# Optimization experiments

Hardware: AMD Instinct MI355X
Metric: run time of the kernel (lower is better)

Reference implementation:

```python
import jax, jax.numpy as jnp
import numpy as np


def quat2mat(q):
    # q: [B,4] in (w,x,y,z) order; normalize then standard rotation matrix.
    q = q / jnp.linalg.norm(q, axis=-1, keepdims=True)
    w, x, y, z = q[:, 0], q[:, 1], q[:, 2], q[:, 3]
    R = jnp.stack([
        1 - 2 * (y * y + z * z), 2 * (x * y - w * z), 2 * (x * z + w * y),
        2 * (x * y + w * z), 1 - 2 * (x * x + z * z), 2 * (y * z - w * x),
        2 * (x * z - w * y), 2 * (y * z + w * x), 1 - 2 * (x * x + y * y),
    ], axis=-1).reshape(-1, 3, 3)
    return R


def setup_inputs() -> dict:
    key = jax.random.key(0)
    k1, k2, k3, k4, k5 = jax.random.split(key, 5)
    B, N = 32, 2048
    return {
        "q_est": jax.random.normal(k1, (B, 4), dtype=jnp.float32),
        "q_gt": jax.random.normal(k2, (B, 4), dtype=jnp.float32),
        "T": jax.random.normal(k3, (B, 3), dtype=jnp.float32),
        "pts": jax.random.normal(k4, (B, N, 3), dtype=jnp.float32),
        "symmetries": jax.random.randint(k5, (B, 1), 0, 2, dtype=jnp.int32),
    }


def reference(q_est, q_gt, T, pts, symmetries):
    # ego=False path: T unused.
    B = pts.shape[0]
    N = pts.shape[1]
    sym = symmetries.reshape(-1).astype(bool)  # [B]

    R_est = quat2mat(q_est)  # [B,3,3]
    R_gt = quat2mat(q_gt)

    pts_t = jnp.transpose(pts, (0, 2, 1))        # [B,3,N]
    pts_est = R_est @ pts_t                       # [B,3,N]
    pts_gt = R_gt @ pts_t                         # [B,3,N]

    # PLoss per-point squared distances: [B,N]
    d_p = jnp.sum((pts_est - pts_gt) ** 2, axis=1)

    # SLoss: pairwise squared dists via bmm decomposition, then min over gt points.
    x = jnp.transpose(pts_est, (0, 2, 1))  # [B,N,3]
    y = jnp.transpose(pts_gt, (0, 2, 1))   # [B,N,3]
    xx = jnp.sum(x * x, axis=-1)           # [B,N] (diag of x x^T)
    yy = jnp.sum(y * y, axis=-1)           # [B,N]
    zz = jnp.einsum('bnd,bmd->bnm', x, y)  # [B,N,N]
    P = xx[:, :, None] + yy[:, None, :] - 2.0 * zz
    d_s = jnp.min(P, axis=2)               # [B,N]

    # num_sym * s_loss / size + num_non_sym * p_loss / size simplifies to
    # (masked_sum_s + masked_sum_p) / (2 * N * B); num_sym/num_non_sym cancel.
    sum_s = jnp.sum(jnp.where(sym[:, None], d_s, 0.0))
    sum_p = jnp.sum(jnp.where(sym[:, None], 0.0, d_p))
    return (sum_s + sum_p) / (2.0 * N * B)
```

## Files before the change

kernel.cpp:

```cpp
#include <hip/hip_runtime.h>


#define TPB  256
#define NPTS 2048
#define MS   16
#define MCH  (NPTS / MS)
#define PX   8

__device__ __forceinline__ void quat2mat(const float* __restrict__ q, float R[9]) {
    float w = q[0], x = q[1], y = q[2], z = q[3];
    float inv = 1.0f / sqrtf(w*w + x*x + y*y + z*z);
    w *= inv; x *= inv; y *= inv; z *= inv;
    R[0] = 1.f - 2.f*(y*y + z*z); R[1] = 2.f*(x*y - w*z);       R[2] = 2.f*(x*z + w*y);
    R[3] = 2.f*(x*y + w*z);       R[4] = 1.f - 2.f*(x*x + z*z); R[5] = 2.f*(y*z - w*x);
    R[6] = 2.f*(x*z - w*y);       R[7] = 2.f*(y*z + w*x);       R[8] = 1.f - 2.f*(x*x + y*y);
}

__device__ __forceinline__ float block_reduce_add(float v, float* red) {
    #pragma unroll
    for (int off = 32; off > 0; off >>= 1)
        v += __shfl_down(v, off, 64);
    const int tid = threadIdx.x;
    if ((tid & 63) == 0) red[tid >> 6] = v;
    __syncthreads();
    return red[0] + red[1] + red[2] + red[3];
}

__global__ __launch_bounds__(TPB) void pts_loss_A(
    const float* __restrict__ q_est, const float* __restrict__ q_gt,
    const float* __restrict__ pts, const int* __restrict__ symmetries,
    float* __restrict__ out, float* __restrict__ partial,
    float* __restrict__ bsum)
{
    const int b   = blockIdx.x;
    const int ms  = blockIdx.y;
    const int tid = threadIdx.x;

    __shared__ float4 ybuf[MCH];
    __shared__ float  red[TPB / 64];

    if (b == 0 && ms == 0 && tid == 0) *out = 0.f;

    const bool is_sym = symmetries[b] != 0;
    const float* pb = pts + (size_t)b * NPTS * 3;

    if (!is_sym) {
        if (ms != 0) return;
        float Re[9], Rg[9];
        quat2mat(q_est + 4*b, Re);
        quat2mat(q_gt  + 4*b, Rg);
        float s = 0.f;
        #pragma unroll
        for (int k = 0; k < PX; ++k) {
            int n = k * TPB + tid;
            float p0 = pb[3*n+0], p1 = pb[3*n+1], p2 = pb[3*n+2];
            float d0 = (Re[0]-Rg[0])*p0 + (Re[1]-Rg[1])*p1 + (Re[2]-Rg[2])*p2;
            float d1 = (Re[3]-Rg[3])*p0 + (Re[4]-Rg[4])*p1 + (Re[5]-Rg[5])*p2;
            float d2 = (Re[6]-Rg[6])*p0 + (Re[7]-Rg[7])*p1 + (Re[8]-Rg[8])*p2;
            s += d0*d0 + d1*d1 + d2*d2;
        }
        s = block_reduce_add(s, red);
        if (tid == 0) bsum[b] = s;
        return;
    }

    float Re[9], Rg[9];
    quat2mat(q_est + 4*b, Re);
    quat2mat(q_gt  + 4*b, Rg);

    if (tid < MCH) {
        int m = ms * MCH + tid;
        float p0 = pb[3*m+0], p1 = pb[3*m+1], p2 = pb[3*m+2];
        float y0 = Rg[0]*p0 + Rg[1]*p1 + Rg[2]*p2;
        float y1 = Rg[3]*p0 + Rg[4]*p1 + Rg[5]*p2;
        float y2 = Rg[6]*p0 + Rg[7]*p1 + Rg[8]*p2;
        ybuf[tid] = make_float4(y0, y1, y2, y0*y0 + y1*y1 + y2*y2);
    }
    __syncthreads();

    float nx0[PX], nx1[PX], nx2[PX], xx[PX], mins[PX];
    #pragma unroll
    for (int k = 0; k < PX; ++k) {
        int n = k * TPB + tid;
        float p0 = pb[3*n+0], p1 = pb[3*n+1], p2 = pb[3*n+2];
        float x0 = Re[0]*p0 + Re[1]*p1 + Re[2]*p2;
        float x1 = Re[3]*p0 + Re[4]*p1 + Re[5]*p2;
        float x2 = Re[6]*p0 + Re[7]*p1 + Re[8]*p2;
        nx0[k] = -2.f*x0; nx1[k] = -2.f*x1; nx2[k] = -2.f*x2;
        xx[k]  = x0*x0 + x1*x1 + x2*x2;
        mins[k] = 1e30f;
    }

    #pragma unroll 4
    for (int m = 0; m < MCH; ++m) {
        float4 y = ybuf[m];
        #pragma unroll
        for (int k = 0; k < PX; ++k) {
            float t = fmaf(nx0[k], y.x, fmaf(nx1[k], y.y, fmaf(nx2[k], y.z, y.w)));
            mins[k] = fminf(mins[k], t);
        }
    }

    float* pp = partial + ((size_t)b * MS + ms) * NPTS;
    #pragma unroll
    for (int k = 0; k < PX; ++k)
        pp[k * TPB + tid] = mins[k] + xx[k];
}

__global__ __launch_bounds__(TPB) void pts_loss_B(
    const int* __restrict__ symmetries,
    const float* __restrict__ partial,
    const float* __restrict__ bsum, float* __restrict__ out, float scale)
{
    const int b   = blockIdx.x;
    const int tid = threadIdx.x;
    __shared__ float red[TPB / 64];

    if (symmetries[b] == 0) {
        if (tid == 0) atomicAdd(out, bsum[b] * scale);
        return;
    }

    const float* pb = partial + (size_t)b * MS * NPTS;
    float s = 0.f;
    #pragma unroll
    for (int k = 0; k < PX; ++k) {
        int n = k * TPB + tid;
        float v = pb[n];
        #pragma unroll
        for (int ms = 1; ms < MS; ++ms)
            v = fminf(v, pb[ms * NPTS + n]);
        s += v;
    }
    s = block_reduce_add(s, red);
    if (tid == 0) atomicAdd(out, s * scale);
}

extern "C" void kernel_launch(void* const* d_in, const int* in_sizes, int n_in,
                              void* d_out, int out_size, void* d_ws, size_t ws_size,
                              hipStream_t stream) {
    const float* q_est = (const float*)d_in[0];
    const float* q_gt  = (const float*)d_in[1];
    const float* pts   = (const float*)d_in[3];
    const int*   sym   = (const int*)d_in[4];
    float* out = (float*)d_out;

    const int B = in_sizes[0] / 4;
    const float scale = 1.0f / (2.0f * (float)NPTS * (float)B);

    float* partial = (float*)d_ws;
    float* bsum    = partial + (size_t)B * MS * NPTS;

    dim3 gridA(B, MS);
    pts_loss_A<<<gridA, TPB, 0, stream>>>(q_est, q_gt, pts, sym, out, partial, bsum);
    pts_loss_B<<<B, TPB, 0, stream>>>(sym, partial, bsum, out, scale);
}
```

Before: 74.79 us.

## Fuse two-pass chamfer min into single kernel with full gt set in LDS

Each block now owns 128 estimated points and loads all 2048 transformed gt points into 32KB of shared memory, so the min over gt points finishes inside the block. This removes the partial-min workspace write, the second reduction kernel, and one launch. Each thread does 2048 iterations with four independent min chains instead of a register tile of 8 points over 128 y values. Redundancy rises: every block recomputes all gt transforms. Per-thread ALU work and LDS traffic per FMA also go up, and the 32KB of LDS per block may limit occupancy.

```diff
diff --git a/kernel.cpp b/kernel.cpp
--- a/kernel.cpp
+++ b/kernel.cpp
@@ -1,11 +1,12 @@
 #include <hip/hip_runtime.h>
 
 
-#define TPB  256
-#define NPTS 2048
-#define MS   16
-#define MCH  (NPTS / MS)
-#define PX   8
+#define NPTS  2048
+#define NC    16
+#define TPB   128
+#define YPT   (NPTS / TPB)
+
+static_assert(NPTS / NC == TPB, "one x-point per thread");
 
 __device__ __forceinline__ void quat2mat(const float* __restrict__ q, float R[9]) {
     float w = q[0], x = q[1], y = q[2], z = q[3];
@@ -23,115 +24,70 @@
     const int tid = threadIdx.x;
     if ((tid & 63) == 0) red[tid >> 6] = v;
     __syncthreads();
-    return red[0] + red[1] + red[2] + red[3];
+    return red[0] + red[1];
 }
 
-__global__ __launch_bounds__(TPB) void pts_loss_A(
+__global__ __launch_bounds__(TPB) void pts_loss_fused(
     const float* __restrict__ q_est, const float* __restrict__ q_gt,
     const float* __restrict__ pts, const int* __restrict__ symmetries,
-    float* __restrict__ out, float* __restrict__ partial,
-    float* __restrict__ bsum)
+    float* __restrict__ out, float scale)
 {
     const int b   = blockIdx.x;
-    const int ms  = blockIdx.y;
+    const int c   = blockIdx.y;
     const int tid = threadIdx.x;
 
-    __shared__ float4 ybuf[MCH];
+    __shared__ float4 ybuf[NPTS];
     __shared__ float  red[TPB / 64];
-
-    if (b == 0 && ms == 0 && tid == 0) *out = 0.f;
 
     const bool is_sym = symmetries[b] != 0;
     const float* pb = pts + (size_t)b * NPTS * 3;
-
-    if (!is_sym) {
-        if (ms != 0) return;
-        float Re[9], Rg[9];
-        quat2mat(q_est + 4*b, Re);
-        quat2mat(q_gt  + 4*b, Rg);
-        float s = 0.f;
-        #pragma unroll
-        for (int k = 0; k < PX; ++k) {
-            int n = k * TPB + tid;
-            float p0 = pb[3*n+0], p1 = pb[3*n+1], p2 = pb[3*n+2];
-            float d0 = (Re[0]-Rg[0])*p0 + (Re[1]-Rg[1])*p1 + (Re[2]-Rg[2])*p2;
-            float d1 = (Re[3]-Rg[3])*p0 + (Re[4]-Rg[4])*p1 + (Re[5]-Rg[5])*p2;
-            float d2 = (Re[6]-Rg[6])*p0 + (Re[7]-Rg[7])*p1 + (Re[8]-Rg[8])*p2;
-            s += d0*d0 + d1*d1 + d2*d2;
-        }
-        s = block_reduce_add(s, red);
-        if (tid == 0) bsum[b] = s;
-        return;
-    }
 
     float Re[9], Rg[9];
     quat2mat(q_est + 4*b, Re);
     quat2mat(q_gt  + 4*b, Rg);
 
-    if (tid < MCH) {
-        int m = ms * MCH + tid;
-        float p0 = pb[3*m+0], p1 = pb[3*m+1], p2 = pb[3*m+2];
-        float y0 = Rg[0]*p0 + Rg[1]*p1 + Rg[2]*p2;
-        float y1 = Rg[3]*p0 + Rg[4]*p1 + Rg[5]*p2;
-        float y2 = Rg[6]*p0 + Rg[7]*p1 + Rg[8]*p2;
-        ybuf[tid] = make_float4(y0, y1, y2, y0*y0 + y1*y1 + y2*y2);
-    }
-    __syncthreads();
+    const int   n  = c * TPB + tid;
+    const float p0 = pb[3*n+0], p1 = pb[3*n+1], p2 = pb[3*n+2];
 
-    float nx0[PX], nx1[PX], nx2[PX], xx[PX], mins[PX];
-    #pragma unroll
-    for (int k = 0; k < PX; ++k) {
-        int n = k * TPB + tid;
-        float p0 = pb[3*n+0], p1 = pb[3*n+1], p2 = pb[3*n+2];
+    float s;
+    if (!is_sym) {
+        float d0 = (Re[0]-Rg[0])*p0 + (Re[1]-Rg[1])*p1 + (Re[2]-Rg[2])*p2;
+        float d1 = (Re[3]-Rg[3])*p0 + (Re[4]-Rg[4])*p1 + (Re[5]-Rg[5])*p2;
+        float d2 = (Re[6]-Rg[6])*p0 + (Re[7]-Rg[7])*p1 + (Re[8]-Rg[8])*p2;
+        s = d0*d0 + d1*d1 + d2*d2;
+    } else {
+        #pragma unroll
+        for (int k = 0; k < YPT; ++k) {
+            int m = k * TPB + tid;
+            float a0 = pb[3*m+0], a1 = pb[3*m+1], a2 = pb[3*m+2];
+            float y0 = Rg[0]*a0 + Rg[1]*a1 + Rg[2]*a2;
+            float y1 = Rg[3]*a0 + Rg[4]*a1 + Rg[5]*a2;
+            float y2 = Rg[6]*a0 + Rg[7]*a1 + Rg[8]*a2;
+            ybuf[m] = make_float4(y0, y1, y2, y0*y0 + y1*y1 + y2*y2);
+        }
+        __syncthreads();
+
         float x0 = Re[0]*p0 + Re[1]*p1 + Re[2]*p2;
         float x1 = Re[3]*p0 + Re[4]*p1 + Re[5]*p2;
         float x2 = Re[6]*p0 + Re[7]*p1 + Re[8]*p2;
-        nx0[k] = -2.f*x0; nx1[k] = -2.f*x1; nx2[k] = -2.f*x2;
-        xx[k]  = x0*x0 + x1*x1 + x2*x2;
-        mins[k] = 1e30f;
+        float nx0 = -2.f*x0, nx1 = -2.f*x1, nx2 = -2.f*x2;
+        float xx  = x0*x0 + x1*x1 + x2*x2;
+
+        float m0 = 1e30f, m1 = 1e30f, m2 = 1e30f, m3 = 1e30f;
+        #pragma unroll 2
+        for (int m = 0; m < NPTS; m += 4) {
+            float4 ya = ybuf[m+0];
+            float4 yb = ybuf[m+1];
+            float4 yc = ybuf[m+2];
+            float4 yd = ybuf[m+3];
+            m0 = fminf(m0, fmaf(nx0, ya.x, fmaf(nx1, ya.y, fmaf(nx2, ya.z, ya.w))));
+            m1 = fminf(m1, fmaf(nx0, yb.x, fmaf(nx1, yb.y, fmaf(nx2, yb.z, yb.w))));
+            m2 = fminf(m2, fmaf(nx0, yc.x, fmaf(nx1, yc.y, fmaf(nx2, yc.z, yc.w))));
+            m3 = fminf(m3, fmaf(nx0, yd.x, fmaf(nx1, yd.y, fmaf(nx2, yd.z, yd.w))));
+        }
+        s = xx + fminf(fminf(m0, m1), fminf(m2, m3));
     }
 
-    #pragma unroll 4
-    for (int m = 0; m < MCH; ++m) {
-        float4 y = ybuf[m];
-        #pragma unroll
-        for (int k = 0; k < PX; ++k) {
-            float t = fmaf(nx0[k], y.x, fmaf(nx1[k], y.y, fmaf(nx2[k], y.z, y.w)));
-            mins[k] = fminf(mins[k], t);
-        }
-    }
-
-    float* pp = partial + ((size_t)b * MS + ms) * NPTS;
-    #pragma unroll
-    for (int k = 0; k < PX; ++k)
-        pp[k * TPB + tid] = mins[k] + xx[k];
-}
-
-__global__ __launch_bounds__(TPB) void pts_loss_B(
-    const int* __restrict__ symmetries,
-    const float* __restrict__ partial,
-    const float* __restrict__ bsum, float* __restrict__ out, float scale)
-{
-    const int b   = blockIdx.x;
-    const int tid = threadIdx.x;
-    __shared__ float red[TPB / 64];
-
-    if (symmetries[b] == 0) {
-        if (tid == 0) atomicAdd(out, bsum[b] * scale);
-        return;
-    }
-
-    const float* pb = partial + (size_t)b * MS * NPTS;
-    float s = 0.f;
-    #pragma unroll
-    for (int k = 0; k < PX; ++k) {
-        int n = k * TPB + tid;
-        float v = pb[n];
-        #pragma unroll
-        for (int ms = 1; ms < MS; ++ms)
-            v = fminf(v, pb[ms * NPTS + n]);
-        s += v;
-    }
     s = block_reduce_add(s, red);
     if (tid == 0) atomicAdd(out, s * scale);
 }
@@ -148,10 +104,7 @@
     const int B = in_sizes[0] / 4;
     const float scale = 1.0f / (2.0f * (float)NPTS * (float)B);
 
-    float* partial = (float*)d_ws;
-    float* bsum    = partial + (size_t)B * MS * NPTS;
-
-    dim3 gridA(B, MS);
-    pts_loss_A<<<gridA, TPB, 0, stream>>>(q_est, q_gt, pts, sym, out, partial, bsum);
-    pts_loss_B<<<B, TPB, 0, stream>>>(sym, partial, bsum, out, scale);
+    hipMemsetAsync(out, 0, sizeof(float), stream);
+    dim3 grid(B, NC);
+    pts_loss_fused<<<grid, TPB, 0, stream>>>(q_est, q_gt, pts, sym, out, scale);
 }
```

Measured after the change: 92.44 us. +23.6%, slower.
